# Performance work log

Measured on AMD Instinct MI355X. Metric: run time of the kernel, lower is better.

## Reference

```python
import jax, jax.numpy as jnp
import numpy as np

N_Q = 10           # qubits
N_BLOCKS = 10      # encoding blocks (== N_Q so adjoint start-index arithmetic matches source)
DIM = 1 << N_Q     # 1024 state-vector dimension
P = 128            # number of data points -> P*P pairwise circuit evaluations

SQRT2 = np.float32(np.sqrt(2.0))

# bits[d, q] = q-th bit (MSB-first) of basis index d
_bits_np = ((np.arange(DIM)[:, None] >> (N_Q - 1 - np.arange(N_Q))) & 1).astype(np.float32)
BITS = jnp.asarray(_bits_np)  # [DIM, N_Q]
# CRZ-ring diagonal feature: control q, target (q+1) % N_Q; phase exp(1j*theta_q*s_q*(s_{q+1}-1/2))
RING = jnp.asarray(_bits_np * (np.roll(_bits_np, -1, axis=1) - 0.5))  # [DIM, N_Q]


def _apply_1q(state, U, q):
    # state: [B, DIM]; apply 2x2 U to qubit q (MSB-first ordering)
    B = state.shape[0]
    s = state.reshape(B, 1 << q, 2, 1 << (N_Q - q - 1))
    s = jnp.einsum('ij,bajc->baic', U, s)
    return s.reshape(B, DIM)


def h_layer(state):
    H = jnp.asarray([[1, 1], [1, -1]], dtype=state.dtype) / SQRT2
    for q in range(N_Q):
        state = _apply_1q(state, H, q)
    return state


def rz_layer(state, thetas):
    # thetas: [B, N_Q] per-pair data angles; RZ(t) = diag(e^{-it/2}, e^{it/2})
    phases = jnp.exp(1j * jnp.einsum('dq,bq->bd', BITS - 0.5, thetas))
    return state * phases.astype(state.dtype)


def ry_layer(state, thetas):
    # thetas: [N_Q] shared trainable angles
    for q in range(N_Q):
        c, s = jnp.cos(thetas[q] / 2), jnp.sin(thetas[q] / 2)
        U = jnp.stack([jnp.stack([c, -s]), jnp.stack([s, c])]).astype(state.dtype)
        state = _apply_1q(state, U, q)
    return state


def crz_ring(state, thetas):
    # entire CRZ ring is diagonal in the computational basis -> single fused multiply
    phases = jnp.exp(1j * (RING @ thetas))  # [DIM]
    return state * phases.astype(state.dtype)


def circuit(x1, x2, params):
    # x1, x2: [B, N_BLOCKS*N_Q]; params: [N_BLOCKS, 2, N_Q]
    B = x1.shape[0]
    state = jnp.zeros((B, DIM), jnp.complex64).at[:, 0].set(1.0)
    for j in range(N_BLOCKS):  # block(...)
        state = h_layer(state)
        state = rz_layer(state, x1[:, j * N_Q:(j + 1) * N_Q])
        state = ry_layer(state, params[j, 0])
        state = crz_ring(state, params[j, 1])
    for k in range(N_BLOCKS):  # adj_block(...) over reversed(params)
        bp = params[N_BLOCKS - 1 - k]
        start = (N_Q - k - 1) * N_Q  # exactly as written in the source
        state = crz_ring(state, -bp[1])   # adjoint of diagonal gate = negated angles
        state = ry_layer(state, -bp[0])   # RY(-t); single-qubit gates commute across qubits
        state = rz_layer(state, -x2[:, start:start + N_Q])
        state = h_layer(state)            # H is self-adjoint
    return state


def setup_inputs() -> dict:
    key = jax.random.key(0)
    k1, k2, k3 = jax.random.split(key, 3)
    data = jax.random.normal(k1, (P, N_BLOCKS * N_Q), jnp.float32)
    labels = jnp.sign(jax.random.normal(k2, (P,), jnp.float32))  # +/-1 class labels
    params = jax.random.normal(k3, (N_BLOCKS, 2, N_Q), jnp.float32)
    return {"data": data, "labels": labels, "params": params}


def reference(data, labels, params):
    # k_fusion: kernel-target-alignment over all (i, j) pairs, fully batched
    n = data.shape[0]
    x1 = jnp.repeat(data, n, axis=0)   # point i for each pair (pair-major)
    x2 = jnp.tile(data, (n, 1))        # point j for each pair
    state = circuit(x1, x2, params)
    K = (jnp.abs(state[:, 0]) ** 2).reshape(n, n)  # probability of |0...0>
    ll = labels[:, None] * labels[None, :]
    polarity = jnp.sum(ll * K)
    norm = jnp.sqrt(jnp.sum(K ** 2) * jnp.sum(ll ** 2))
    return polarity / norm
```

## Files before the change

### kernel.cpp

```cpp
#include <hip/hip_runtime.h>
#include <math.h>

#define NQ   10
#define DIM  1024
#define NB   10
#define NPTS 128
#define S2   0.70710678118654752440f

__device__ __forceinline__ void cmul_ph(float& vr, float& vi, float ph) {
    float s, c;
    __sincosf(ph, &s, &c);
    const float ar = vr, ai = vi;
    vr = ar * c - ai * s;
    vi = ar * s + ai * c;
}

#define H_PAIR(i0, i1) {                                   \
    const float ar = vr[i0], ai = vi[i0];                  \
    const float br = vr[i1], bi = vi[i1];                  \
    vr[i0] = (ar + br) * S2;  vi[i0] = (ai + bi) * S2;     \
    vr[i1] = (ar - br) * S2;  vi[i1] = (ai - bi) * S2; }

#define RY_PAIR(i0, i1, c, s) {                            \
    const float ar = vr[i0], ai = vi[i0];                  \
    const float br = vr[i1], bi = vi[i1];                  \
    vr[i0] = c * ar - s * br;  vi[i0] = c * ai - s * bi;   \
    vr[i1] = s * ar + c * br;  vi[i1] = s * ai + c * bi; }

__global__ __launch_bounds__(256)
void states_kernel(const float* __restrict__ data,
                   const float* __restrict__ params,
                   float2* __restrict__ psi,
                   double* __restrict__ acc)
{
    __shared__ float sRe[DIM];
    __shared__ float sIm[DIM];

    const int tid  = threadIdx.x;
    const int w    = tid >> 6;
    const int lane = tid & 63;
    const int pt   = blockIdx.x;

    const int cbase = w * 256 + lane * 4;
    const int tb    = lane * 4 + w;

    if (pt == 0 && tid == 0) { acc[0] = 0.0; acc[1] = 0.0; }

    float vr[4], vi[4];
    vr[0] = vr[1] = vr[2] = vr[3] = 0.f;
    vi[0] = vi[1] = vi[2] = vi[3] = 0.f;
    if (tid == 0) vr[0] = 1.f;

    const float* x = data + pt * (NB * NQ);

    for (int j = 0; j < NB; ++j) {
        const float* ry  = params + j * 2 * NQ;
        const float* crz = ry + NQ;
        const float* xb  = x + j * NQ;

        H_PAIR(0, 2) H_PAIR(1, 3)
        H_PAIR(0, 1) H_PAIR(2, 3)
        #pragma unroll
        for (int l = 0; l < 6; ++l) {
            const float sg = ((lane >> l) & 1) ? -1.f : 1.f;
            #pragma unroll
            for (int r = 0; r < 4; ++r) {
                const float ur = __shfl_xor(vr[r], 1 << l, 64);
                const float ui = __shfl_xor(vi[r], 1 << l, 64);
                vr[r] = (ur + sg * vr[r]) * S2;
                vi[r] = (ui + sg * vi[r]) * S2;
            }
        }
        __syncthreads();
        *(float4*)&sRe[cbase] = make_float4(vr[0], vr[1], vr[2], vr[3]);
        *(float4*)&sIm[cbase] = make_float4(vi[0], vi[1], vi[2], vi[3]);
        __syncthreads();
        #pragma unroll
        for (int k = 0; k < 4; ++k) { vr[k] = sRe[k * 256 + tb]; vi[k] = sIm[k * 256 + tb]; }
        H_PAIR(0, 2) H_PAIR(1, 3)
        H_PAIR(0, 1) H_PAIR(2, 3)

        {
            const float x0 = xb[0], x1 = xb[1];
            float base_ph = -0.5f * (x0 + x1);
            #pragma unroll
            for (int q = 2; q < NQ; ++q)
                base_ph += (((tb >> (9 - q)) & 1) - 0.5f) * xb[q];
            cmul_ph(vr[0], vi[0], base_ph);
            cmul_ph(vr[1], vi[1], base_ph + x1);
            cmul_ph(vr[2], vi[2], base_ph + x0);
            cmul_ph(vr[3], vi[3], base_ph + x0 + x1);
        }

        {
            float c, s;
            __sincosf(ry[0] * 0.5f, &s, &c);
            RY_PAIR(0, 2, c, s) RY_PAIR(1, 3, c, s)
            __sincosf(ry[1] * 0.5f, &s, &c);
            RY_PAIR(0, 1, c, s) RY_PAIR(2, 3, c, s)
        }
        #pragma unroll
        for (int l = 0; l < 6; ++l) {
            float c, s;
            __sincosf(ry[7 - l] * 0.5f, &s, &c);
            const float ss = ((lane >> l) & 1) ? s : -s;
            #pragma unroll
            for (int r = 0; r < 4; ++r) {
                const float ur = __shfl_xor(vr[r], 1 << l, 64);
                const float ui = __shfl_xor(vi[r], 1 << l, 64);
                vr[r] = c * vr[r] + ss * ur;
                vi[r] = c * vi[r] + ss * ui;
            }
        }
        __syncthreads();
        #pragma unroll
        for (int k = 0; k < 4; ++k) { sRe[k * 256 + tb] = vr[k]; sIm[k * 256 + tb] = vi[k]; }
        __syncthreads();
        {
            const float4 fr = *(const float4*)&sRe[cbase];
            const float4 fi = *(const float4*)&sIm[cbase];
            vr[0] = fr.x; vr[1] = fr.y; vr[2] = fr.z; vr[3] = fr.w;
            vi[0] = fi.x; vi[1] = fi.y; vi[2] = fi.z; vi[3] = fi.w;
        }
        {
            float c, s;
            __sincosf(ry[8] * 0.5f, &s, &c);
            RY_PAIR(0, 2, c, s) RY_PAIR(1, 3, c, s)
            __sincosf(ry[9] * 0.5f, &s, &c);
            RY_PAIR(0, 1, c, s) RY_PAIR(2, 3, c, s)
        }

        {
            const int hb = (w << 6) | lane;
            float common = 0.f;
            #pragma unroll
            for (int q = 0; q <= 6; ++q) {
                const float bq  = (float)((hb >> (7 - q)) & 1);
                const float bq1 = (float)((hb >> (6 - q)) & 1);
                common += crz[q] * bq * (bq1 - 0.5f);
            }
            const float b2 = (float)(hb & 1);
            const float b9 = (float)((hb >> 7) & 1);
            const float t7 = crz[7], t8 = crz[8], t9 = crz[9];
            #pragma unroll
            for (int r = 0; r < 4; ++r) {
                const float r1 = (float)((r >> 1) & 1);
                const float r0 = (float)(r & 1);
                const float ph = common
                               + t7 * b2 * (r1 - 0.5f)
                               + t8 * r1 * (r0 - 0.5f)
                               + t9 * r0 * (b9 - 0.5f);
                cmul_ph(vr[r], vi[r], ph);
            }
        }
    }

    float2* out = psi + pt * DIM + cbase;
    *(float4*)&out[0] = make_float4(vr[0], vi[0], vr[1], vi[1]);
    *(float4*)&out[2] = make_float4(vr[2], vi[2], vr[3], vi[3]);
}

#define TS 32
#define KC 64
#define KSPLIT (DIM / KC)

__global__ __launch_bounds__(256)
void gram_kernel(const float2* __restrict__ psi, float2* __restrict__ Gpart)
{
    __shared__ float2 A [TS][KC + 2];
    __shared__ float2 Bt[KC][TS + 2];

    const int tid  = threadIdx.x;
    const int bx   = blockIdx.x;
    const int ks   = bx & 15;
    const int tile = bx >> 4;
    const int ti   = tile >> 2, tj = tile & 3;
    const int kbase = ks * KC;

    #pragma unroll
    for (int it = 0; it < 2; ++it) {
        const int slot = it * 256 + tid;
        const int row  = slot >> 4;
        const int kq   = (slot & 15) << 2;
        const float4* sa = (const float4*)(psi + (ti * TS + row) * DIM + kbase + kq);
        const float4 a01 = sa[0], a23 = sa[1];
        *(float4*)&A[row][kq]     = a01;
        *(float4*)&A[row][kq + 2] = a23;
        const float4* sb = (const float4*)(psi + (tj * TS + row) * DIM + kbase + kq);
        const float4 b01 = sb[0], b23 = sb[1];
        Bt[kq + 0][row] = make_float2(b01.x, b01.y);
        Bt[kq + 1][row] = make_float2(b01.z, b01.w);
        Bt[kq + 2][row] = make_float2(b23.x, b23.y);
        Bt[kq + 3][row] = make_float2(b23.z, b23.w);
    }
    __syncthreads();

    const int ty = tid >> 4, tx = tid & 15;
    float g00r = 0.f, g00i = 0.f, g01r = 0.f, g01i = 0.f;
    float g10r = 0.f, g10i = 0.f, g11r = 0.f, g11i = 0.f;

    #pragma unroll 4
    for (int k = 0; k < KC; k += 2) {
        const float4 a0 = *(const float4*)&A[2 * ty    ][k];
        const float4 a1 = *(const float4*)&A[2 * ty + 1][k];
        const float4 b0 = *(const float4*)&Bt[k    ][2 * tx];
        const float4 b1 = *(const float4*)&Bt[k + 1][2 * tx];
        g00r += a0.x * b0.x + a0.y * b0.y;  g00i += a0.x * b0.y - a0.y * b0.x;
        g01r += a0.x * b0.z + a0.y * b0.w;  g01i += a0.x * b0.w - a0.y * b0.z;
        g10r += a1.x * b0.x + a1.y * b0.y;  g10i += a1.x * b0.y - a1.y * b0.x;
        g11r += a1.x * b0.z + a1.y * b0.w;  g11i += a1.x * b0.w - a1.y * b0.z;
        g00r += a0.z * b1.x + a0.w * b1.y;  g00i += a0.z * b1.y - a0.w * b1.x;
        g01r += a0.z * b1.z + a0.w * b1.w;  g01i += a0.z * b1.w - a0.w * b1.z;
        g10r += a1.z * b1.x + a1.w * b1.y;  g10i += a1.z * b1.y - a1.w * b1.x;
        g11r += a1.z * b1.z + a1.w * b1.w;  g11i += a1.z * b1.w - a1.w * b1.z;
    }

    float2* gp = Gpart + ks * (NPTS * NPTS);
    const int gr0 = ti * TS + 2 * ty, gc0 = tj * TS + 2 * tx;
    gp[(gr0    ) * NPTS + gc0    ] = make_float2(g00r, g00i);
    gp[(gr0    ) * NPTS + gc0 + 1] = make_float2(g01r, g01i);
    gp[(gr0 + 1) * NPTS + gc0    ] = make_float2(g10r, g10i);
    gp[(gr0 + 1) * NPTS + gc0 + 1] = make_float2(g11r, g11i);
}

__global__ __launch_bounds__(256)
void reduce_kernel(const float2* __restrict__ Gpart,
                   const float* __restrict__ labels,
                   double* __restrict__ acc)
{
    const int idx = blockIdx.x * 256 + threadIdx.x;
    float gr = 0.f, gi = 0.f;
    #pragma unroll
    for (int p = 0; p < KSPLIT; ++p) {
        const float2 g = Gpart[p * (NPTS * NPTS) + idx];
        gr += g.x; gi += g.y;
    }
    const int i  = idx >> 7;
    const int jj = idx & (NPTS - 1);
    const float K = gr * gr + gi * gi;
    double pol = (double)(labels[i] * labels[jj]) * (double)K;
    double k2  = (double)K * (double)K;
    #pragma unroll
    for (int off = 32; off > 0; off >>= 1) {
        pol += __shfl_xor(pol, off, 64);
        k2  += __shfl_xor(k2,  off, 64);
    }
    __shared__ double sp[4], sk[4];
    const int wv = threadIdx.x >> 6;
    if ((threadIdx.x & 63) == 0) { sp[wv] = pol; sk[wv] = k2; }
    __syncthreads();
    if (threadIdx.x == 0) {
        atomicAdd(&acc[0], sp[0] + sp[1] + sp[2] + sp[3]);
        atomicAdd(&acc[1], sk[0] + sk[1] + sk[2] + sk[3]);
    }
}

__global__ void finalize_kernel(const double* __restrict__ acc,
                                const float* __restrict__ labels,
                                float* __restrict__ out)
{
    double sumL2 = 0.0;
    for (int i = 0; i < NPTS; ++i) {
        const double l = (double)labels[i];
        sumL2 += l * l;
    }
    out[0] = (float)(acc[0] / (sumL2 * sqrt(acc[1])));
}

extern "C" void kernel_launch(void* const* d_in, const int* in_sizes, int n_in,
                              void* d_out, int out_size, void* d_ws, size_t ws_size,
                              hipStream_t stream)
{
    const float* data   = (const float*)d_in[0];
    const float* labels = (const float*)d_in[1];
    const float* params = (const float*)d_in[2];
    float* out = (float*)d_out;

    float2* psi   = (float2*)d_ws;
    float2* Gpart = (float2*)((char*)d_ws + (size_t)(1u << 20));
    double* acc   = (double*)((char*)d_ws + (size_t)(3u << 20));

    states_kernel<<<NPTS, 256, 0, stream>>>(data, params, psi, acc);
    gram_kernel<<<TS ? 256 : 0, 256, 0, stream>>>(psi, Gpart);
    reduce_kernel<<<(NPTS * NPTS) / 256, 256, 0, stream>>>(Gpart, labels, acc);
    finalize_kernel<<<1, 1, 0, stream>>>(acc, labels, out);
}
```

Before: 98.33 us.

## Fuse gram, reduce and finalize into one row kernel; double-buffer shared state

Replaces the tiled split-K Gram kernel, the partial-sum reduce kernel and the single-thread finalize kernel with one kernel. Each block computes one row of overlaps, reduces it, and the last block (found through an atomic counter) writes the final alignment value. This removes two launches and the round trip of the partial Gram buffer through global memory. The states kernel also gets separate shared buffers for its two transposes, so two barriers per block go away. The cost is a gram kernel that reads every psi row straight from global or L2 memory without tiling reuse, and that depends on the counter reset done in the previous kernel.

```diff
diff --git a/kernel.cpp b/kernel.cpp
--- a/kernel.cpp
+++ b/kernel.cpp
@@ -31,10 +31,13 @@
 void states_kernel(const float* __restrict__ data,
                    const float* __restrict__ params,
                    float2* __restrict__ psi,
-                   double* __restrict__ acc)
+                   double* __restrict__ acc,
+                   int* __restrict__ cnt)
 {
-    __shared__ float sRe[DIM];
-    __shared__ float sIm[DIM];
+    __shared__ float aRe[DIM];
+    __shared__ float aIm[DIM];
+    __shared__ float bRe[DIM];
+    __shared__ float bIm[DIM];
 
     const int tid  = threadIdx.x;
     const int w    = tid >> 6;
@@ -44,7 +47,7 @@
     const int cbase = w * 256 + lane * 4;
     const int tb    = lane * 4 + w;
 
-    if (pt == 0 && tid == 0) { acc[0] = 0.0; acc[1] = 0.0; }
+    if (pt == 0 && tid == 0) { acc[0] = 0.0; acc[1] = 0.0; cnt[0] = 0; }
 
     float vr[4], vi[4];
     vr[0] = vr[1] = vr[2] = vr[3] = 0.f;
@@ -71,12 +74,11 @@
                 vi[r] = (ui + sg * vi[r]) * S2;
             }
         }
+        *(float4*)&aRe[cbase] = make_float4(vr[0], vr[1], vr[2], vr[3]);
+        *(float4*)&aIm[cbase] = make_float4(vi[0], vi[1], vi[2], vi[3]);
         __syncthreads();
-        *(float4*)&sRe[cbase] = make_float4(vr[0], vr[1], vr[2], vr[3]);
-        *(float4*)&sIm[cbase] = make_float4(vi[0], vi[1], vi[2], vi[3]);
-        __syncthreads();
-        #pragma unroll
-        for (int k = 0; k < 4; ++k) { vr[k] = sRe[k * 256 + tb]; vi[k] = sIm[k * 256 + tb]; }
+        #pragma unroll
+        for (int k = 0; k < 4; ++k) { vr[k] = aRe[k * 256 + tb]; vi[k] = aIm[k * 256 + tb]; }
         H_PAIR(0, 2) H_PAIR(1, 3)
         H_PAIR(0, 1) H_PAIR(2, 3)
 
@@ -112,13 +114,12 @@
                 vi[r] = c * vi[r] + ss * ui;
             }
         }
+        #pragma unroll
+        for (int k = 0; k < 4; ++k) { bRe[k * 256 + tb] = vr[k]; bIm[k * 256 + tb] = vi[k]; }
         __syncthreads();
-        #pragma unroll
-        for (int k = 0; k < 4; ++k) { sRe[k * 256 + tb] = vr[k]; sIm[k * 256 + tb] = vi[k]; }
-        __syncthreads();
-        {
-            const float4 fr = *(const float4*)&sRe[cbase];
-            const float4 fi = *(const float4*)&sIm[cbase];
+        {
+            const float4 fr = *(const float4*)&bRe[cbase];
+            const float4 fi = *(const float4*)&bIm[cbase];
             vr[0] = fr.x; vr[1] = fr.y; vr[2] = fr.z; vr[3] = fr.w;
             vi[0] = fi.x; vi[1] = fi.y; vi[2] = fi.z; vi[3] = fi.w;
         }
@@ -160,111 +161,73 @@
     *(float4*)&out[2] = make_float4(vr[2], vi[2], vr[3], vi[3]);
 }
 
-#define TS 32
-#define KC 64
-#define KSPLIT (DIM / KC)
-
 __global__ __launch_bounds__(256)
-void gram_kernel(const float2* __restrict__ psi, float2* __restrict__ Gpart)
+void gramrow_kernel(const float2* __restrict__ psi,
+                    const float* __restrict__ labels,
+                    double* __restrict__ acc,
+                    int* __restrict__ cnt,
+                    float* __restrict__ out)
 {
-    __shared__ float2 A [TS][KC + 2];
-    __shared__ float2 Bt[KC][TS + 2];
-
-    const int tid  = threadIdx.x;
-    const int bx   = blockIdx.x;
-    const int ks   = bx & 15;
-    const int tile = bx >> 4;
-    const int ti   = tile >> 2, tj = tile & 3;
-    const int kbase = ks * KC;
-
+    __shared__ float4 sA[DIM / 2];
+    __shared__ double sp[4], sk[4];
+
+    const int i   = blockIdx.x;
+    const int tid = threadIdx.x;
+
+    const float4* rowi = (const float4*)(psi + (size_t)i * DIM);
     #pragma unroll
-    for (int it = 0; it < 2; ++it) {
-        const int slot = it * 256 + tid;
-        const int row  = slot >> 4;
-        const int kq   = (slot & 15) << 2;
-        const float4* sa = (const float4*)(psi + (ti * TS + row) * DIM + kbase + kq);
-        const float4 a01 = sa[0], a23 = sa[1];
-        *(float4*)&A[row][kq]     = a01;
-        *(float4*)&A[row][kq + 2] = a23;
-        const float4* sb = (const float4*)(psi + (tj * TS + row) * DIM + kbase + kq);
-        const float4 b01 = sb[0], b23 = sb[1];
-        Bt[kq + 0][row] = make_float2(b01.x, b01.y);
-        Bt[kq + 1][row] = make_float2(b01.z, b01.w);
-        Bt[kq + 2][row] = make_float2(b23.x, b23.y);
-        Bt[kq + 3][row] = make_float2(b23.z, b23.w);
-    }
+    for (int t = tid; t < DIM / 2; t += 256) sA[t] = rowi[t];
     __syncthreads();
 
-    const int ty = tid >> 4, tx = tid & 15;
-    float g00r = 0.f, g00i = 0.f, g01r = 0.f, g01i = 0.f;
-    float g10r = 0.f, g10i = 0.f, g11r = 0.f, g11i = 0.f;
-
-    #pragma unroll 4
-    for (int k = 0; k < KC; k += 2) {
-        const float4 a0 = *(const float4*)&A[2 * ty    ][k];
-        const float4 a1 = *(const float4*)&A[2 * ty + 1][k];
-        const float4 b0 = *(const float4*)&Bt[k    ][2 * tx];
-        const float4 b1 = *(const float4*)&Bt[k + 1][2 * tx];
-        g00r += a0.x * b0.x + a0.y * b0.y;  g00i += a0.x * b0.y - a0.y * b0.x;
-        g01r += a0.x * b0.z + a0.y * b0.w;  g01i += a0.x * b0.w - a0.y * b0.z;
-        g10r += a1.x * b0.x + a1.y * b0.y;  g10i += a1.x * b0.y - a1.y * b0.x;
-        g11r += a1.x * b0.z + a1.y * b0.w;  g11i += a1.x * b0.w - a1.y * b0.z;
-        g00r += a0.z * b1.x + a0.w * b1.y;  g00i += a0.z * b1.y - a0.w * b1.x;
-        g01r += a0.z * b1.z + a0.w * b1.w;  g01i += a0.z * b1.w - a0.w * b1.z;
-        g10r += a1.z * b1.x + a1.w * b1.y;  g10i += a1.z * b1.y - a1.w * b1.x;
-        g11r += a1.z * b1.z + a1.w * b1.w;  g11i += a1.z * b1.w - a1.w * b1.z;
-    }
-
-    float2* gp = Gpart + ks * (NPTS * NPTS);
-    const int gr0 = ti * TS + 2 * ty, gc0 = tj * TS + 2 * tx;
-    gp[(gr0    ) * NPTS + gc0    ] = make_float2(g00r, g00i);
-    gp[(gr0    ) * NPTS + gc0 + 1] = make_float2(g01r, g01i);
-    gp[(gr0 + 1) * NPTS + gc0    ] = make_float2(g10r, g10i);
-    gp[(gr0 + 1) * NPTS + gc0 + 1] = make_float2(g11r, g11i);
-}
-
-__global__ __launch_bounds__(256)
-void reduce_kernel(const float2* __restrict__ Gpart,
-                   const float* __restrict__ labels,
-                   double* __restrict__ acc)
-{
-    const int idx = blockIdx.x * 256 + threadIdx.x;
+    const int j   = tid >> 1;
+    const int sub = tid & 1;
+    const float4* rowj = (const float4*)(psi + (size_t)j * DIM) + sub * (DIM / 4);
+    const float4* ai   = sA + sub * (DIM / 4);
+
     float gr = 0.f, gi = 0.f;
+    #pragma unroll 8
+    for (int t = 0; t < DIM / 4; ++t) {
+        const float4 a = ai[t];
+        const float4 b = rowj[t];
+        gr += a.x * b.x + a.y * b.y;
+        gi += a.x * b.y - a.y * b.x;
+        gr += a.z * b.z + a.w * b.w;
+        gi += a.z * b.w - a.w * b.z;
+    }
+    gr += __shfl_xor(gr, 1, 64);
+    gi += __shfl_xor(gi, 1, 64);
+
+    double pol = 0.0, k2 = 0.0;
+    if (sub == 0) {
+        const float K  = gr * gr + gi * gi;
+        const float ll = labels[i] * labels[j];
+        pol = (double)(ll * K);
+        k2  = (double)K * (double)K;
+    }
     #pragma unroll
-    for (int p = 0; p < KSPLIT; ++p) {
-        const float2 g = Gpart[p * (NPTS * NPTS) + idx];
-        gr += g.x; gi += g.y;
-    }
-    const int i  = idx >> 7;
-    const int jj = idx & (NPTS - 1);
-    const float K = gr * gr + gi * gi;
-    double pol = (double)(labels[i] * labels[jj]) * (double)K;
-    double k2  = (double)K * (double)K;
-    #pragma unroll
-    for (int off = 32; off > 0; off >>= 1) {
+    for (int off = 1; off < 64; off <<= 1) {
         pol += __shfl_xor(pol, off, 64);
         k2  += __shfl_xor(k2,  off, 64);
     }
-    __shared__ double sp[4], sk[4];
-    const int wv = threadIdx.x >> 6;
-    if ((threadIdx.x & 63) == 0) { sp[wv] = pol; sk[wv] = k2; }
+    const int wv = tid >> 6;
+    if ((tid & 63) == 0) { sp[wv] = pol; sk[wv] = k2; }
     __syncthreads();
-    if (threadIdx.x == 0) {
+    if (tid == 0) {
         atomicAdd(&acc[0], sp[0] + sp[1] + sp[2] + sp[3]);
         atomicAdd(&acc[1], sk[0] + sk[1] + sk[2] + sk[3]);
-    }
-}
-
-__global__ void finalize_kernel(const double* __restrict__ acc,
-                                const float* __restrict__ labels,
-                                float* __restrict__ out)
-{
-    double sumL2 = 0.0;
-    for (int i = 0; i < NPTS; ++i) {
-        const double l = (double)labels[i];
-        sumL2 += l * l;
-    }
-    out[0] = (float)(acc[0] / (sumL2 * sqrt(acc[1])));
+        __threadfence();
+        const int done = atomicAdd(cnt, 1);
+        if (done == NPTS - 1) {
+            const double p  = atomicAdd(&acc[0], 0.0);
+            const double s2 = atomicAdd(&acc[1], 0.0);
+            double sumL2 = 0.0;
+            for (int t = 0; t < NPTS; ++t) {
+                const double l = (double)labels[t];
+                sumL2 += l * l;
+            }
+            out[0] = (float)(p / (sumL2 * sqrt(s2)));
+        }
+    }
 }
 
 extern "C" void kernel_launch(void* const* d_in, const int* in_sizes, int n_in,
@@ -276,12 +239,10 @@
     const float* params = (const float*)d_in[2];
     float* out = (float*)d_out;
 
-    float2* psi   = (float2*)d_ws;
-    float2* Gpart = (float2*)((char*)d_ws + (size_t)(1u << 20));
-    double* acc   = (double*)((char*)d_ws + (size_t)(3u << 20));
-
-    states_kernel<<<NPTS, 256, 0, stream>>>(data, params, psi, acc);
-    gram_kernel<<<TS ? 256 : 0, 256, 0, stream>>>(psi, Gpart);
-    reduce_kernel<<<(NPTS * NPTS) / 256, 256, 0, stream>>>(Gpart, labels, acc);
-    finalize_kernel<<<1, 1, 0, stream>>>(acc, labels, out);
-}
+    float2* psi = (float2*)d_ws;
+    double* acc = (double*)((char*)d_ws + (size_t)(1u << 20));
+    int*    cnt = (int*)   ((char*)d_ws + (size_t)(1u << 20) + 16);
+
+    states_kernel<<<NPTS, 256, 0, stream>>>(data, params, psi, acc, cnt);
+    gramrow_kernel<<<NPTS, 256, 0, stream>>>(psi, labels, acc, cnt, out);
+}
```

Result: slower. 127.4 us (+29.6%).
